# Performance work log

Hardware: AMD Instinct MI355X
Metric: run time of the kernel (lower is better)

## Reference

```python
import jax, jax.numpy as jnp
import numpy as np

B, N, D, ATT = 8, 2048, 1024, 128

def setup_inputs() -> dict:
    key = jax.random.key(0)
    k1, k2, k3 = jax.random.split(key, 3)
    s = 1.0 / np.sqrt(D)
    return {
        "x": jax.random.normal(k1, (B, N, D), dtype=jnp.float32),
        "Wf": jax.random.normal(k2, (D, ATT), dtype=jnp.float32) * s,
        "bf": jnp.zeros((ATT,), dtype=jnp.float32),
        "Wg": jax.random.normal(k3, (D, ATT), dtype=jnp.float32) * s,
        "bg": jnp.zeros((ATT,), dtype=jnp.float32),
    }

def reference(x, Wf, bf, Wg, bg):
    # f, g: [B, N, ATT]
    f = jnp.einsum('bnd,da->bna', x, Wf) + bf
    g = jnp.einsum('bnd,da->bna', x, Wg) + bg
    # unscaled attention logits [B, N, N]
    att = jnp.einsum('bna,bma->bnm', f, g)
    att = jax.nn.softmax(att, axis=-1)
    # NOTE: original multiplies attention with x (not h); h branch is dead code.
    out = jnp.einsum('bnm,bmd->bnd', att, x)
    return out + x  # residual=True
```

## Files before the change

kernel.cpp:

```cpp
#include <hip/hip_runtime.h>
#include <hip/hip_fp16.h>


#define B_ 8
#define N_ 2048
#define D_ 1024
#define A_ 128

typedef _Float16 half8v  __attribute__((ext_vector_type(8)));
typedef _Float16 half4v  __attribute__((ext_vector_type(4)));
typedef short    short8v __attribute__((ext_vector_type(8)));
typedef float    floatx4 __attribute__((ext_vector_type(4)));

#define SOFT_C 44.0f

__device__ __forceinline__ floatx4 mfma32(half8v a, half8v b, floatx4 c) {
#if defined(__HIP_DEVICE_COMPILE__)
    return __builtin_amdgcn_mfma_f32_16x16x32_f16(a, b, c, 0, 0, 0);
#else
    return c;
#endif
}
__device__ __forceinline__ floatx4 mfma32bf(short8v a, short8v b, floatx4 c) {
#if defined(__HIP_DEVICE_COMPILE__)
    return __builtin_amdgcn_mfma_f32_16x16x32_bf16(a, b, c, 0, 0, 0);
#else
    return c;
#endif
}

__device__ __forceinline__ unsigned short f2bf(float x) {
    union { float f; unsigned int u; } v; v.f = x;
    unsigned int u = v.u + 0x7fffu + ((v.u >> 16) & 1u);
    return (unsigned short)(u >> 16);
}

__device__ __forceinline__ void gload_lds16(const void* gsrc, void* ldst) {
#if defined(__HIP_DEVICE_COMPILE__)
    __builtin_amdgcn_global_load_lds(
        (const __attribute__((address_space(1))) void*)gsrc,
        (__attribute__((address_space(3))) void*)ldst, 16, 0, 0);
#endif
}

__global__ __launch_bounds__(256) void xpose_kernel(
    const float* __restrict__ x, unsigned short* __restrict__ xT)
{
    __shared__ __align__(16) unsigned short ts[64][80];
    const int n0 = blockIdx.x * 64, d0 = blockIdx.y * 64, b = blockIdx.z;
    const int t = threadIdx.x;
#pragma unroll
    for (int s = 0; s < 4; ++s) {
        int idx = t + 256 * s;
        int nl = idx >> 4, c4 = idx & 15;
        float4 v = ((const float4*)(x + ((size_t)(b * N_ + n0 + nl)) * D_ + d0))[c4];
        ts[c4 * 4 + 0][nl] = f2bf(v.x);
        ts[c4 * 4 + 1][nl] = f2bf(v.y);
        ts[c4 * 4 + 2][nl] = f2bf(v.z);
        ts[c4 * 4 + 3][nl] = f2bf(v.w);
    }
    __syncthreads();
#pragma unroll
    for (int s = 0; s < 2; ++s) {
        int idx = t + 256 * s;
        int dl = idx >> 3, c = idx & 7;
        *(uint4*)&xT[((size_t)b * D_ + d0 + dl) * N_ + n0 + c * 8] =
            *(const uint4*)&ts[dl][c * 8];
    }
}

__global__ __launch_bounds__(256) void wprep_kernel(
    const float* __restrict__ Wf, const float* __restrict__ Wg,
    _Float16* __restrict__ whT)
{
    __shared__ __align__(16) _Float16 ts[64][72];
    const int k0 = blockIdx.x * 64, c0 = blockIdx.y * 64;
    const float* W = blockIdx.z ? Wg : Wf;
    _Float16* dst = whT + (size_t)blockIdx.z * A_ * D_;
    const int t = threadIdx.x;
#pragma unroll
    for (int s = 0; s < 4; ++s) {
        int idx = t + 256 * s;
        int kl = idx >> 4, c4 = idx & 15;
        float4 v = *(const float4*)&W[(size_t)(k0 + kl) * A_ + c0 + c4 * 4];
        ts[c4 * 4 + 0][kl] = (_Float16)v.x;
        ts[c4 * 4 + 1][kl] = (_Float16)v.y;
        ts[c4 * 4 + 2][kl] = (_Float16)v.z;
        ts[c4 * 4 + 3][kl] = (_Float16)v.w;
    }
    __syncthreads();
#pragma unroll
    for (int s = 0; s < 2; ++s) {
        int idx = t + 256 * s;
        int cl = idx >> 3, ch = idx & 7;
        *(uint4*)&dst[(size_t)(c0 + cl) * D_ + k0 + ch * 8] =
            *(const uint4*)&ts[cl][ch * 8];
    }
}

__global__ __launch_bounds__(256) void fgmm_kernel(
    const float* __restrict__ x, const _Float16* __restrict__ whT,
    const float* __restrict__ bfv, const float* __restrict__ bgv,
    _Float16* __restrict__ fh, _Float16* __restrict__ gh)
{
    __shared__ __align__(16) _Float16 xs[64 * 40];
    __shared__ __align__(16) _Float16 wt[256 * 40];
    const int row0 = blockIdx.x * 64;
    const int t = threadIdx.x;
    const int w = t >> 6, lane = t & 63, quad = lane >> 4, l16 = lane & 15;
    const int wr  = (w >> 1) * 32;
    const int wch = (w & 1);

    float4 xRf[2];
    uint4  wR[4];
#define FG_LOAD_TILE(K0)                                                      \
    {                                                                         \
        _Pragma("unroll")                                                     \
        for (int s = 0; s < 2; ++s) {                                         \
            int idx = t + 256 * s;                                            \
            int r = idx >> 3, k4 = idx & 7;                                   \
            xRf[s] = *(const float4*)&x[(size_t)(row0 + r) * D_ + (K0) + k4 * 4]; \
        }                                                                     \
        _Pragma("unroll")                                                     \
        for (int s = 0; s < 4; ++s) {                                         \
            int idx = t + 256 * s;                                            \
            int c = idx >> 2, k8 = idx & 3;                                   \
            wR[s] = *(const uint4*)&whT[(size_t)c * D_ + (K0) + k8 * 8];      \
        }                                                                     \
    }

    FG_LOAD_TILE(0)

    floatx4 acc[2][8];
#pragma unroll
    for (int ms = 0; ms < 2; ++ms)
#pragma unroll
        for (int nt = 0; nt < 8; ++nt)
            acc[ms][nt] = (floatx4){0.f, 0.f, 0.f, 0.f};

    for (int kt = 0; kt < 32; ++kt) {
        __syncthreads();
#pragma unroll
        for (int s = 0; s < 2; ++s) {
            int idx = t + 256 * s;
            int r = idx >> 3, k4 = idx & 7;
            half4v h = {(_Float16)xRf[s].x, (_Float16)xRf[s].y,
                        (_Float16)xRf[s].z, (_Float16)xRf[s].w};
            *(half4v*)&xs[r * 40 + k4 * 4] = h;
        }
#pragma unroll
        for (int s = 0; s < 4; ++s) {
            int idx = t + 256 * s;
            int c = idx >> 2, k8 = idx & 3;
            *(uint4*)&wt[c * 40 + k8 * 8] = wR[s];
        }
        __syncthreads();
        if (kt < 31) FG_LOAD_TILE((kt + 1) * 32)

        half8v a0 = *(const half8v*)&xs[(wr + l16) * 40 + quad * 8];
        half8v a1 = *(const half8v*)&xs[(wr + 16 + l16) * 40 + quad * 8];
#pragma unroll
        for (int nt = 0; nt < 8; ++nt) {
            half8v bfr = *(const half8v*)&wt[(wch * 128 + nt * 16 + l16) * 40 + quad * 8];
            acc[0][nt] = mfma32(a0, bfr, acc[0][nt]);
            acc[1][nt] = mfma32(a1, bfr, acc[1][nt]);
        }
    }

    _Float16* dst = wch ? gh : fh;
    const float* bias = wch ? bgv : bfv;
#pragma unroll
    for (int nt = 0; nt < 8; ++nt) {
        int col = nt * 16 + l16;
        float bv = bias[col];
#pragma unroll
        for (int ms = 0; ms < 2; ++ms)
#pragma unroll
            for (int rg = 0; rg < 4; ++rg) {
                int row = row0 + wr + ms * 16 + quad * 4 + rg;
                dst[(size_t)row * A_ + col] = (_Float16)(acc[ms][nt][rg] + bv);
            }
    }
}

__global__ __launch_bounds__(256) void attp_kernel(
    const _Float16* __restrict__ f, const _Float16* __restrict__ g,
    unsigned short* __restrict__ P, float* __restrict__ lsum)
{
    __shared__ __align__(16) unsigned short tps[4][16 * 56];
    __shared__ float lred[4][16];

    const int tid = threadIdx.x;
    const int wave = tid >> 6, lane = tid & 63;
    const int quad = lane >> 4, l16 = lane & 15;
    const int q0 = blockIdx.x * 16;
    const int b  = blockIdx.y;
    const int kbase = wave * 512;

    half8v fb[4];
#pragma unroll
    for (int kc = 0; kc < 4; ++kc)
        fb[kc] = *(const half8v*)(f +
            ((size_t)(b * N_ + q0 + l16)) * A_ + kc * 32 + quad * 8);

    unsigned short* slab = &tps[wave][0];
    float l_part = 0.f;

#define ATTP_LOADG(A0, A1, M0)                                                \
    {                                                                         \
        _Pragma("unroll")                                                     \
        for (int kc = 0; kc < 4; ++kc) {                                      \
            A0[kc] = *(const half8v*)(g +                                     \
                ((size_t)(b * N_ + (M0) + l16)) * A_ + kc * 32 + quad * 8);   \
            A1[kc] = *(const half8v*)(g +                                     \
                ((size_t)(b * N_ + (M0) + 16 + l16)) * A_ + kc * 32 + quad * 8); \
        }                                                                     \
    }

#define ATTP_COMPUTE(A0, A1, TT)                                              \
    {                                                                         \
        const int m0 = kbase + (TT) * 32;                                     \
        floatx4 sc0 = (floatx4){0.f, 0.f, 0.f, 0.f};                          \
        floatx4 sc1 = (floatx4){0.f, 0.f, 0.f, 0.f};                          \
        _Pragma("unroll")                                                     \
        for (int kc = 0; kc < 4; ++kc) {                                      \
            sc0 = mfma32(A0[kc], fb[kc], sc0);                                \
            sc1 = mfma32(A1[kc], fb[kc], sc1);                                \
        }                                                                     \
        float e0 = __expf(sc0[0] - SOFT_C), e1 = __expf(sc0[1] - SOFT_C);     \
        float e2 = __expf(sc0[2] - SOFT_C), e3 = __expf(sc0[3] - SOFT_C);     \
        float e4 = __expf(sc1[0] - SOFT_C), e5 = __expf(sc1[1] - SOFT_C);     \
        float e6 = __expf(sc1[2] - SOFT_C), e7 = __expf(sc1[3] - SOFT_C);     \
        l_part += ((e0 + e1) + (e2 + e3)) + ((e4 + e5) + (e6 + e7));          \
        unsigned int w01 = (unsigned int)f2bf(e0) | ((unsigned int)f2bf(e1) << 16); \
        unsigned int w23 = (unsigned int)f2bf(e2) | ((unsigned int)f2bf(e3) << 16); \
        unsigned int w45 = (unsigned int)f2bf(e4) | ((unsigned int)f2bf(e5) << 16); \
        unsigned int w67 = (unsigned int)f2bf(e6) | ((unsigned int)f2bf(e7) << 16); \
        *(unsigned int*)&slab[l16 * 56 + quad * 4]          = w01;            \
        *(unsigned int*)&slab[l16 * 56 + quad * 4 + 2]      = w23;            \
        *(unsigned int*)&slab[l16 * 56 + 16 + quad * 4]     = w45;            \
        *(unsigned int*)&slab[l16 * 56 + 16 + quad * 4 + 2] = w67;            \
        asm volatile("s_waitcnt lgkmcnt(0)" ::: "memory");                    \
        __builtin_amdgcn_sched_barrier(0);                                    \
        uint4 pvv = *(const uint4*)&slab[(lane >> 2) * 56 + (lane & 3) * 8];  \
        *(uint4*)(P + ((size_t)(b * N_ + q0 + (lane >> 2))) * N_ +            \
                  m0 + (lane & 3) * 8) = pvv;                                 \
    }

    half8v ga0[4], ga1[4], gb0[4], gb1[4];
    ATTP_LOADG(ga0, ga1, kbase)
#pragma unroll 1
    for (int tp = 0; tp < 8; ++tp) {
        ATTP_LOADG(gb0, gb1, kbase + (tp * 2 + 1) * 32)
        ATTP_COMPUTE(ga0, ga1, tp * 2)
        if (tp < 7) ATTP_LOADG(ga0, ga1, kbase + (tp * 2 + 2) * 32)
        ATTP_COMPUTE(gb0, gb1, tp * 2 + 1)
    }

    l_part += __shfl_xor(l_part, 16);
    l_part += __shfl_xor(l_part, 32);
    if (lane < 16) lred[wave][lane] = l_part;
    __syncthreads();
    if (wave == 0 && lane < 16)
        lsum[(size_t)b * N_ + q0 + lane] =
            (lred[0][lane] + lred[1][lane]) + (lred[2][lane] + lred[3][lane]);
}

__global__ __launch_bounds__(512, 4) void pv_kernel(
    const unsigned short* __restrict__ P, const unsigned short* __restrict__ xT,
    const float* __restrict__ lsum, const float* __restrict__ x,
    float* __restrict__ out)
{
    __shared__ __align__(16) unsigned short Ps[3][128 * 32];
    __shared__ __align__(16) unsigned short Xs[3][256 * 32];

    const int bm = blockIdx.x;
    const int dn = blockIdx.y;
    const int b  = blockIdx.z;
    const int tid = threadIdx.x;
    const int wave = tid >> 6, lane = tid & 63;
    const int quad = lane >> 4, l16 = lane & 15;
    const int wm = wave >> 2, wn = wave & 3;
    const int chq = (quad ^ ((l16 >> 1) & 3)) * 8;

#define PV_STAGE(BUF, T0)                                                     \
    {                                                                         \
        {                                                                     \
            int row = tid >> 2, c = tid & 3;                                  \
            int cc = c ^ ((row >> 1) & 3);                                    \
            gload_lds16(P + ((size_t)(b * N_ + bm * 128 + row)) * N_ +        \
                            (T0) + cc * 8,                                    \
                        &Ps[BUF][(wave * 64) * 8]);                           \
        }                                                                     \
        _Pragma("unroll")                                                     \
        for (int s = 0; s < 2; ++s) {                                         \
            int idx = s * 512 + tid;                                          \
            int row = idx >> 2, c = idx & 3;                                  \
            int cc = c ^ ((row >> 1) & 3);                                    \
            gload_lds16(xT + ((size_t)(b * D_ + dn * 256 + row)) * N_ +       \
                            (T0) + cc * 8,                                    \
                        &Xs[BUF][(s * 512 + wave * 64) * 8]);                 \
        }                                                                     \
    }

    floatx4 acc[4][4];
#pragma unroll
    for (int m = 0; m < 4; ++m)
#pragma unroll
        for (int n = 0; n < 4; ++n)
            acc[m][n] = (floatx4){0.f, 0.f, 0.f, 0.f};

    PV_STAGE(0, 0)
    PV_STAGE(1, 32)
    asm volatile("s_waitcnt vmcnt(3)" ::: "memory");
    __builtin_amdgcn_sched_barrier(0);
    __builtin_amdgcn_s_barrier();

    int cur = 0;
    for (int t = 0; t < 64; ++t) {
        int nx2 = cur + 2; if (nx2 >= 3) nx2 -= 3;
        if (t < 62) PV_STAGE(nx2, (t + 2) * 32)

        short8v a[4], bb[4];
#pragma unroll
        for (int m = 0; m < 4; ++m)
            a[m] = *(const short8v*)&Ps[cur][(wm * 64 + m * 16 + l16) * 32 + chq];
#pragma unroll
        for (int n = 0; n < 4; ++n)
            bb[n] = *(const short8v*)&Xs[cur][(wn * 64 + n * 16 + l16) * 32 + chq];

        __builtin_amdgcn_s_setprio(1);
#pragma unroll
        for (int m = 0; m < 4; ++m)
#pragma unroll
            for (int n = 0; n < 4; ++n)
                acc[m][n] = mfma32bf(a[m], bb[n], acc[m][n]);
        __builtin_amdgcn_s_setprio(0);

        if (t < 63) {
            asm volatile("s_waitcnt lgkmcnt(0)" ::: "memory");
            if (t < 62) {
                asm volatile("s_waitcnt vmcnt(3)" ::: "memory");
            } else {
                asm volatile("s_waitcnt vmcnt(0)" ::: "memory");
            }
            __builtin_amdgcn_sched_barrier(0);
            __builtin_amdgcn_s_barrier();
            __builtin_amdgcn_sched_barrier(0);
        }
        cur = (cur == 2) ? 0 : cur + 1;
    }

    float linv[4];
#pragma unroll
    for (int m = 0; m < 4; ++m) {
#pragma unroll
        for (int rg = 0; rg < 4; ++rg) {
            int row = bm * 128 + wm * 64 + m * 16 + quad * 4 + rg;
            linv[rg] = 1.0f / lsum[(size_t)b * N_ + row];
            const size_t rowoff = ((size_t)(b * N_ + row)) * D_ + dn * 256;
#pragma unroll
            for (int n = 0; n < 4; ++n) {
                int col = wn * 64 + n * 16 + l16;
                out[rowoff + col] =
                    fmaf(acc[m][n][rg], linv[rg], x[rowoff + col]);
            }
        }
    }
}

extern "C" void kernel_launch(void* const* d_in, const int* in_sizes, int n_in,
                              void* d_out, int out_size, void* d_ws, size_t ws_size,
                              hipStream_t stream) {
    const float* x   = (const float*)d_in[0];
    const float* Wf  = (const float*)d_in[1];
    const float* bfv = (const float*)d_in[2];
    const float* Wg  = (const float*)d_in[3];
    const float* bgv = (const float*)d_in[4];
    float* out = (float*)d_out;

    _Float16*       fh  = (_Float16*)d_ws;
    _Float16*       gh  = fh + (size_t)B_ * N_ * A_;
    unsigned short* xT  = (unsigned short*)(gh + (size_t)B_ * N_ * A_);
    _Float16*       whT = (_Float16*)(xT + (size_t)B_ * D_ * N_);
    unsigned short* P   = (unsigned short*)(whT + (size_t)2 * A_ * D_);
    float*          lsum = (float*)(P + (size_t)B_ * N_ * N_);

    hipLaunchKernelGGL(xpose_kernel, dim3(N_ / 64, D_ / 64, B_), dim3(256), 0, stream,
                       x, xT);
    hipLaunchKernelGGL(wprep_kernel, dim3(D_ / 64, A_ / 64, 2), dim3(256), 0, stream,
                       Wf, Wg, whT);
    hipLaunchKernelGGL(fgmm_kernel, dim3(B_ * N_ / 64), dim3(256), 0, stream,
                       x, whT, bfv, bgv, fh, gh);
    hipLaunchKernelGGL(attp_kernel, dim3(N_ / 16, B_), dim3(256), 0, stream,
                       fh, gh, P, lsum);
    hipLaunchKernelGGL(pv_kernel, dim3(N_ / 128, D_ / 256, B_), dim3(512), 0, stream,
                       P, xT, lsum, x, out);
}
```

Before: 313.7 us.

## Permute P and xT column layouts to drop LDS staging; widen fgmm to 512 threads

```diff
diff --git a/kernel.cpp b/kernel.cpp
--- a/kernel.cpp
+++ b/kernel.cpp
@@ -63,9 +63,12 @@
 #pragma unroll
     for (int s = 0; s < 2; ++s) {
         int idx = t + 256 * s;
-        int dl = idx >> 3, c = idx & 7;
-        *(uint4*)&xT[((size_t)b * D_ + d0 + dl) * N_ + n0 + c * 8] =
-            *(const uint4*)&ts[dl][c * 8];
+        int dl = idx >> 3, p = idx & 7;
+        int T = p >> 2, pp = p & 3;
+        uint2 lo = *(const uint2*)&ts[dl][T * 32 + pp * 4];
+        uint2 hi = *(const uint2*)&ts[dl][T * 32 + 16 + pp * 4];
+        uint4 v4 = {lo.x, lo.y, hi.x, hi.y};
+        *(uint4*)&xT[((size_t)b * D_ + d0 + dl) * N_ + n0 + p * 8] = v4;
     }
 }
 
@@ -98,7 +101,7 @@
     }
 }
 
-__global__ __launch_bounds__(256) void fgmm_kernel(
+__global__ __launch_bounds__(512) void fgmm_kernel(
     const float* __restrict__ x, const _Float16* __restrict__ whT,
     const float* __restrict__ bfv, const float* __restrict__ bgv,
     _Float16* __restrict__ fh, _Float16* __restrict__ gh)
@@ -108,22 +111,20 @@
     const int row0 = blockIdx.x * 64;
     const int t = threadIdx.x;
     const int w = t >> 6, lane = t & 63, quad = lane >> 4, l16 = lane & 15;
-    const int wr  = (w >> 1) * 32;
+    const int wr  = (w >> 1) * 16;
     const int wch = (w & 1);
 
-    float4 xRf[2];
-    uint4  wR[4];
+    float4 xRf;
+    uint4  wR[2];
 #define FG_LOAD_TILE(K0)                                                      \
     {                                                                         \
+        {                                                                     \
+            int r = t >> 3, k4 = t & 7;                                       \
+            xRf = *(const float4*)&x[(size_t)(row0 + r) * D_ + (K0) + k4 * 4];\
+        }                                                                     \
         _Pragma("unroll")                                                     \
         for (int s = 0; s < 2; ++s) {                                         \
-            int idx = t + 256 * s;                                            \
-            int r = idx >> 3, k4 = idx & 7;                                   \
-            xRf[s] = *(const float4*)&x[(size_t)(row0 + r) * D_ + (K0) + k4 * 4]; \
-        }                                                                     \
-        _Pragma("unroll")                                                     \
-        for (int s = 0; s < 4; ++s) {                                         \
-            int idx = t + 256 * s;                                            \
+            int idx = t + 512 * s;                                            \
             int c = idx >> 2, k8 = idx & 3;                                   \
             wR[s] = *(const uint4*)&whT[(size_t)c * D_ + (K0) + k8 * 8];      \
         }                                                                     \
@@ -131,26 +132,22 @@
 
     FG_LOAD_TILE(0)
 
-    floatx4 acc[2][8];
-#pragma unroll
-    for (int ms = 0; ms < 2; ++ms)
-#pragma unroll
-        for (int nt = 0; nt < 8; ++nt)
-            acc[ms][nt] = (floatx4){0.f, 0.f, 0.f, 0.f};
+    floatx4 acc[8];
+#pragma unroll
+    for (int nt = 0; nt < 8; ++nt)
+        acc[nt] = (floatx4){0.f, 0.f, 0.f, 0.f};
 
     for (int kt = 0; kt < 32; ++kt) {
         __syncthreads();
+        {
+            int r = t >> 3, k4 = t & 7;
+            half4v h = {(_Float16)xRf.x, (_Float16)xRf.y,
+                        (_Float16)xRf.z, (_Float16)xRf.w};
+            *(half4v*)&xs[r * 40 + k4 * 4] = h;
+        }
 #pragma unroll
         for (int s = 0; s < 2; ++s) {
-            int idx = t + 256 * s;
-            int r = idx >> 3, k4 = idx & 7;
-            half4v h = {(_Float16)xRf[s].x, (_Float16)xRf[s].y,
-                        (_Float16)xRf[s].z, (_Float16)xRf[s].w};
-            *(half4v*)&xs[r * 40 + k4 * 4] = h;
-        }
-#pragma unroll
-        for (int s = 0; s < 4; ++s) {
-            int idx = t + 256 * s;
+            int idx = t + 512 * s;
             int c = idx >> 2, k8 = idx & 3;
             *(uint4*)&wt[c * 40 + k8 * 8] = wR[s];
         }
@@ -158,12 +155,10 @@
         if (kt < 31) FG_LOAD_TILE((kt + 1) * 32)
 
         half8v a0 = *(const half8v*)&xs[(wr + l16) * 40 + quad * 8];
-        half8v a1 = *(const half8v*)&xs[(wr + 16 + l16) * 40 + quad * 8];
 #pragma unroll
         for (int nt = 0; nt < 8; ++nt) {
             half8v bfr = *(const half8v*)&wt[(wch * 128 + nt * 16 + l16) * 40 + quad * 8];
-            acc[0][nt] = mfma32(a0, bfr, acc[0][nt]);
-            acc[1][nt] = mfma32(a1, bfr, acc[1][nt]);
+            acc[nt] = mfma32(a0, bfr, acc[nt]);
         }
     }
 
@@ -174,12 +169,10 @@
         int col = nt * 16 + l16;
         float bv = bias[col];
 #pragma unroll
-        for (int ms = 0; ms < 2; ++ms)
-#pragma unroll
-            for (int rg = 0; rg < 4; ++rg) {
-                int row = row0 + wr + ms * 16 + quad * 4 + rg;
-                dst[(size_t)row * A_ + col] = (_Float16)(acc[ms][nt][rg] + bv);
-            }
+        for (int rg = 0; rg < 4; ++rg) {
+            int row = row0 + wr + quad * 4 + rg;
+            dst[(size_t)row * A_ + col] = (_Float16)(acc[nt][rg] + bv);
+        }
     }
 }
 
@@ -187,7 +180,6 @@
     const _Float16* __restrict__ f, const _Float16* __restrict__ g,
     unsigned short* __restrict__ P, float* __restrict__ lsum)
 {
-    __shared__ __align__(16) unsigned short tps[4][16 * 56];
     __shared__ float lred[4][16];
 
     const int tid = threadIdx.x;
@@ -203,7 +195,6 @@
         fb[kc] = *(const half8v*)(f +
             ((size_t)(b * N_ + q0 + l16)) * A_ + kc * 32 + quad * 8);
 
-    unsigned short* slab = &tps[wave][0];
     float l_part = 0.f;
 
 #define ATTP_LOADG(A0, A1, M0)                                                \
@@ -232,19 +223,12 @@
         float e4 = __expf(sc1[0] - SOFT_C), e5 = __expf(sc1[1] - SOFT_C);     \
         float e6 = __expf(sc1[2] - SOFT_C), e7 = __expf(sc1[3] - SOFT_C);     \
         l_part += ((e0 + e1) + (e2 + e3)) + ((e4 + e5) + (e6 + e7));          \
-        unsigned int w01 = (unsigned int)f2bf(e0) | ((unsigned int)f2bf(e1) << 16); \
-        unsigned int w23 = (unsigned int)f2bf(e2) | ((unsigned int)f2bf(e3) << 16); \
-        unsigned int w45 = (unsigned int)f2bf(e4) | ((unsigned int)f2bf(e5) << 16); \
-        unsigned int w67 = (unsigned int)f2bf(e6) | ((unsigned int)f2bf(e7) << 16); \
-        *(unsigned int*)&slab[l16 * 56 + quad * 4]          = w01;            \
-        *(unsigned int*)&slab[l16 * 56 + quad * 4 + 2]      = w23;            \
-        *(unsigned int*)&slab[l16 * 56 + 16 + quad * 4]     = w45;            \
-        *(unsigned int*)&slab[l16 * 56 + 16 + quad * 4 + 2] = w67;            \
-        asm volatile("s_waitcnt lgkmcnt(0)" ::: "memory");                    \
-        __builtin_amdgcn_sched_barrier(0);                                    \
-        uint4 pvv = *(const uint4*)&slab[(lane >> 2) * 56 + (lane & 3) * 8];  \
-        *(uint4*)(P + ((size_t)(b * N_ + q0 + (lane >> 2))) * N_ +            \
-                  m0 + (lane & 3) * 8) = pvv;                                 \
+        uint4 pw = {                                                          \
+            (unsigned int)f2bf(e0) | ((unsigned int)f2bf(e1) << 16),          \
+            (unsigned int)f2bf(e2) | ((unsigned int)f2bf(e3) << 16),          \
+            (unsigned int)f2bf(e4) | ((unsigned int)f2bf(e5) << 16),          \
+            (unsigned int)f2bf(e6) | ((unsigned int)f2bf(e7) << 16)};         \
+        *(uint4*)(P + ((size_t)(b * N_ + q0 + l16)) * N_ + m0 + quad * 8) = pw;\
     }
 
     half8v ga0[4], ga1[4], gb0[4], gb1[4];
@@ -390,7 +374,7 @@
                        x, xT);
     hipLaunchKernelGGL(wprep_kernel, dim3(D_ / 64, A_ / 64, 2), dim3(256), 0, stream,
                        Wf, Wg, whT);
-    hipLaunchKernelGGL(fgmm_kernel, dim3(B_ * N_ / 64), dim3(256), 0, stream,
+    hipLaunchKernelGGL(fgmm_kernel, dim3(B_ * N_ / 64), dim3(512), 0, stream,
                        x, whT, bfv, bgv, fh, gh);
     hipLaunchKernelGGL(attp_kernel, dim3(N_ / 16, B_), dim3(256), 0, stream,
                        fh, gh, P, lsum);
```

Result: slower. 322.6 us (+2.8%).
